# Performance work log

Measured on AMD Instinct MI355X. Metric: run time of the kernel, lower is better.

Reference implementation:

```python
import jax, jax.numpy as jnp
from jax import lax
import numpy as np

B, T, IN, H, OUT = 1024, 100, 64, 512, 64


def setup_inputs() -> dict:
    key = jax.random.key(0)
    ks = jax.random.split(key, 16)
    s_in = 1.0 / np.sqrt(IN)
    s_h = 1.0 / np.sqrt(H)
    inp = {
        'coeffs': jax.random.normal(ks[0], (B, T - 1, 4, IN), jnp.float32),
        'times': jnp.linspace(0.0, 1.0, T, dtype=jnp.float32),
        'dW': jax.random.normal(ks[1], (T - 1, B, H), jnp.float32),
        # initial_network: Linear(IN, H)
        'W_init': jax.random.normal(ks[2], (IN, H), jnp.float32) * s_in,
        'b_init': jnp.zeros((H,), jnp.float32),
        # drift MLP f: H -> H -> H
        'Wf1': jax.random.normal(ks[3], (H, H), jnp.float32) * s_h,
        'bf1': jnp.zeros((H,), jnp.float32),
        'Wf2': jax.random.normal(ks[4], (H, H), jnp.float32) * s_h,
        'bf2': jnp.zeros((H,), jnp.float32),
        # diffusion MLP g: H -> H -> H (tanh-bounded, diagonal noise)
        'Wg1': jax.random.normal(ks[5], (H, H), jnp.float32) * s_h,
        'bg1': jnp.zeros((H,), jnp.float32),
        'Wg2': jax.random.normal(ks[6], (H, H), jnp.float32) * s_h,
        'bg2': jnp.zeros((H,), jnp.float32),
        # readout: Tanh -> Linear(H,H) -> ReLU -> Linear(H,OUT)
        'Wl1': jax.random.normal(ks[7], (H, H), jnp.float32) * s_h,
        'bl1': jnp.zeros((H,), jnp.float32),
        'Wl2': jax.random.normal(ks[8], (H, OUT), jnp.float32) * s_h,
        'bl2': jnp.zeros((OUT,), jnp.float32),
    }
    return inp


def reference(coeffs, times, dW, W_init, b_init, Wf1, bf1, Wf2, bf2,
              Wg1, bg1, Wg2, bg2, Wl1, bl1, Wl2, bl2):
    # y0 = X.evaluate(times[0]) == constant coefficient of first spline segment
    x0 = coeffs[:, 0, 0, :]                      # [B, IN]
    y0 = x0 @ W_init + b_init                    # [B, H]

    def f(y):
        return jnp.tanh(y @ Wf1 + bf1) @ Wf2 + bf2

    def g(y):
        return jnp.tanh(jnp.tanh(y @ Wg1 + bg1) @ Wg2 + bg2)

    hs = times[1:] - times[:-1]                  # [T-1], equals dt on uniform grid

    def step(y, inp):
        h, dw = inp
        y_next = y + f(y) * h + g(y) * (jnp.sqrt(h) * dw)
        return y_next, y_next

    _, ys = lax.scan(step, y0, (hs, dW))         # ys: [T-1, B, H]
    z = jnp.concatenate([y0[None], ys], axis=0)  # [T, B, H]
    z = jnp.transpose(z, (1, 0, 2))              # [B, T, H]  (permute(1,0,2))

    # readout: Tanh -> Linear -> ReLU -> Linear
    out = jax.nn.relu(jnp.tanh(z) @ Wl1 + bl1) @ Wl2 + bl2  # [B, T, OUT]
    return out, z
```

## Files before the change

### kernel.cpp

```cpp
#include <hip/hip_runtime.h>
#include <hip/hip_bf16.h>
#include <math.h>

#define DEV __device__ __forceinline__

typedef __attribute__((ext_vector_type(8))) short short8;
typedef __attribute__((ext_vector_type(4))) float f32x4;
typedef __attribute__((ext_vector_type(4))) unsigned int u32x4;

static constexpr int Bsz  = 1024;
static constexpr int T    = 100;
static constexpr int TM1  = 99;
static constexpr int H    = 512;
static constexpr int OUTD = 64;
static constexpr int H2   = 1024;
static constexpr int BT   = Bsz * T;

DEV unsigned short f2bf(float f){
  unsigned int u = __float_as_uint(f);
  u += 0x7fffu + ((u >> 16) & 1u);
  return (unsigned short)(u >> 16);
}
DEV unsigned pack2(float lo, float hi){
  return (unsigned)f2bf(lo) | ((unsigned)f2bf(hi) << 16);
}
DEV float tanh_fast(float x){
  x = fminf(fmaxf(x, -15.f), 15.f);
  float e = __expf(2.f * x);
  return (e - 1.f) / (e + 1.f);
}

#define AISSUE(dst, p) asm volatile("global_load_dwordx4 %0, %1, off sc0 sc1" : "=&v"(dst) : "v"(p) : "memory")
#define PLOAD(dst, p)  asm volatile("global_load_dword %0, %1, off"          : "=&v"(dst) : "v"(p) : "memory")
#define SC_STORE(p, v) asm volatile("global_store_dword %0, %1, off sc0 sc1" :: "v"(p), "v"(v) : "memory")
#define VWAIT(n)       asm volatile("s_waitcnt vmcnt(" #n ")" ::: "memory"); __builtin_amdgcn_sched_barrier(0)

DEV void gbar(unsigned* cnt, unsigned target){
  __syncthreads();
  if (threadIdx.x == 0){
    __hip_atomic_fetch_add(cnt, 1u, __ATOMIC_RELAXED, __HIP_MEMORY_SCOPE_AGENT);
    while (__hip_atomic_load(cnt, __ATOMIC_RELAXED, __HIP_MEMORY_SCOPE_AGENT) < target)
      __builtin_amdgcn_s_sleep(1);
  }
  __syncthreads();
}

__global__ __launch_bounds__(256) void k_prep(const float* __restrict__ Wf1, const float* __restrict__ Wg1,
                                              const float* __restrict__ Wf2, const float* __restrict__ Wg2,
                                              const float* __restrict__ Wl1, const float* __restrict__ Wl2,
                                              unsigned short* __restrict__ W1T, unsigned short* __restrict__ W2T,
                                              unsigned short* __restrict__ Wl1F, unsigned short* __restrict__ Wl2F){
  __shared__ float tl[32][33];
  const float* src; unsigned short* dst; int N; int fmt;
  switch (blockIdx.z){
    case 0: src = Wf1; dst = W1T;             N = 512; fmt = 0; break;
    case 1: src = Wg1; dst = W1T + 512*512;   N = 512; fmt = 0; break;
    case 2: src = Wf2; dst = W2T;             N = 512; fmt = 0; break;
    case 3: src = Wg2; dst = W2T + 512*512;   N = 512; fmt = 0; break;
    case 4: src = Wl1; dst = Wl1F;            N = 512; fmt = 1; break;
    default: src = Wl2; dst = Wl2F;           N = 64;  fmt = 2; break;
  }
  int k0 = blockIdx.x*32, n0 = blockIdx.y*32;
  if (n0 >= N) return;
  int tx = threadIdx.x, ty = threadIdx.y;
  #pragma unroll
  for (int r = 0; r < 4; r++) tl[ty + r*8][tx] = src[(size_t)(k0 + ty + r*8) * N + n0 + tx];
  __syncthreads();
  if (fmt == 0){
    int kpos = k0 + ((tx & 15)*2 + (tx >> 4));
    #pragma unroll
    for (int r = 0; r < 4; r++) dst[(size_t)(n0 + ty + r*8) * 512 + kpos] = f2bf(tl[tx][ty + r*8]);
  } else {
    int k = k0 + tx;
    int Nc = (fmt == 1) ? 512 : 64;
    #pragma unroll
    for (int r = 0; r < 4; r++){
      int col = n0 + ty + r*8;
      size_t idx = (((size_t)(k >> 5)*Nc + col)*4 + ((k >> 3) & 3))*8 + (k & 7);
      dst[idx] = f2bf(tl[tx][ty + r*8]);
    }
  }
}

__global__ void k_zero(unsigned* __restrict__ cnts){
  cnts[threadIdx.x + blockIdx.x*256] = 0u;
}

#define KS1(K, W) \
  VWAIT(W); \
  { short8 a_ = *(short8*)&ap[(K)&7]; \
    p0 = __builtin_amdgcn_mfma_f32_16x16x32_bf16(a_, wb[(K)*2],   p0, 0,0,0); \
    p1 = __builtin_amdgcn_mfma_f32_16x16x32_bf16(a_, wb[(K)*2+1], p1, 0,0,0); } \
  if ((K) < 8) { AISSUE(ap[(K)&7], abase1 + (size_t)((K)+8)*65536); }

#define RUN16_P1 \
  AISSUE(ap[0], abase1);          AISSUE(ap[1], abase1+65536); \
  AISSUE(ap[2], abase1+131072);   AISSUE(ap[3], abase1+196608); \
  AISSUE(ap[4], abase1+262144);   AISSUE(ap[5], abase1+327680); \
  AISSUE(ap[6], abase1+393216);   AISSUE(ap[7], abase1+458752); \
  KS1( 0,7) KS1( 1,7) KS1( 2,7) KS1( 3,7) KS1( 4,7) KS1( 5,7) KS1( 6,7) KS1( 7,7) \
  KS1( 8,7) KS1( 9,6) KS1(10,5) KS1(11,4) KS1(12,3) KS1(13,2) KS1(14,1) KS1(15,0)

#define KS2(K, W) \
  VWAIT(W); \
  { short8 a_  = *(short8*)&ap[(K)&7]; \
    short8 b0_ = *(const short8*)(Wb2 + (K)*4096 + fr*64 + fq*16); \
    short8 b1_ = *(const short8*)(Wb2 + (K)*4096 + 1024 + fr*64 + fq*16); \
    q0 = __builtin_amdgcn_mfma_f32_16x16x32_bf16(a_, b0_, q0, 0,0,0); \
    q1 = __builtin_amdgcn_mfma_f32_16x16x32_bf16(a_, b1_, q1, 0,0,0); } \
  if ((K) < 8) { AISSUE(ap[(K)&7], abase2 + (size_t)((K)+8)*65536); }

#define RUN16_P2 \
  AISSUE(ap[0], abase2);          AISSUE(ap[1], abase2+65536); \
  AISSUE(ap[2], abase2+131072);   AISSUE(ap[3], abase2+196608); \
  AISSUE(ap[4], abase2+262144);   AISSUE(ap[5], abase2+327680); \
  AISSUE(ap[6], abase2+393216);   AISSUE(ap[7], abase2+458752); \
  KS2( 0,7) KS2( 1,7) KS2( 2,7) KS2( 3,7) KS2( 4,7) KS2( 5,7) KS2( 6,7) KS2( 7,7) \
  KS2( 8,7) KS2( 9,6) KS2(10,5) KS2(11,4) KS2(12,3) KS2(13,2) KS2(14,1) KS2(15,0)

__global__ __launch_bounds__(512, 1) void k_scan(
    const float* __restrict__ coeffs, const float* __restrict__ times,
    const float* __restrict__ dW,     const float* __restrict__ W_init,
    const float* __restrict__ b_init,
    const unsigned short* __restrict__ W1T, const unsigned short* __restrict__ W2T,
    const float* __restrict__ bf1, const float* __restrict__ bg1,
    const float* __restrict__ bf2, const float* __restrict__ bg2,
    unsigned short* __restrict__ ygk, unsigned short* __restrict__ uk,
    float* __restrict__ z, unsigned* __restrict__ cnts){
  __shared__ __align__(16) unsigned char W1s[65536];
  __shared__ __align__(16) unsigned char W2s[65536];
  __shared__ __align__(16) float cmb[64*68];
  __shared__ float tms[104];

  const int bid = blockIdx.x, mt = bid & 15, ns = bid >> 4;
  const int m0 = mt*64, n1 = ns*64, n2 = ns*32;
  const int tid = threadIdx.x, lane = tid & 63, w = tid >> 6;
  const int fr = lane & 15, fq = lane >> 4;
  const int band = w & 3, isg = w >> 2;
  unsigned* cnt = cnts + mt*32;
  unsigned ep = 0;

  #pragma unroll
  for (int i = 0; i < 8; i++){
    int u = i*512 + tid;
    int fqi = u & 3, cl = (u >> 2) & 63, kc = u >> 8;
    *(uint4*)(W1s + (size_t)u*16) = *(const uint4*)(W1T + (size_t)(n1+cl)*512 + kc*32 + fqi*8);
    const unsigned short* s2 = (cl < 32) ? (W2T + (size_t)(n2+cl)*512)
                                         : (W2T + (size_t)262144 + (size_t)(n2+cl-32)*512);
    *(uint4*)(W2s + (size_t)u*16) = *(const uint4*)(s2 + kc*32 + fqi*8);
  }
  if (tid < 100) tms[tid] = times[tid];
  { int row = tid >> 3, c0 = (tid & 7)*8;
    const float* src = coeffs + (size_t)(m0+row)*(TM1*4*64) + c0;
    *(float4*)(&cmb[row*68 + c0])     = *(const float4*)src;
    *(float4*)(&cmb[row*68 + c0 + 4]) = *(const float4*)(src + 4);
  }
  __syncthreads();

  short8 wb[32];
  #pragma unroll
  for (int kc = 0; kc < 16; ++kc){
    wb[kc*2]   = *(const short8*)(W1s + kc*4096 + isg*2048 +        fr*64 + fq*16);
    wb[kc*2+1] = *(const short8*)(W1s + kc*4096 + isg*2048 + 1024 + fr*64 + fq*16);
  }

  char* ygkb = (char*)ygk;
  char* ukb  = (char*)uk;
  const char* abase1 = ygkb + ((size_t)(m0 + band*16 + fr))*64 + fq*16;
  const char* abase2 = ukb + (size_t)isg*1048576 + ((size_t)(m0 + band*16 + fr))*64 + fq*16;
  char* ust = ukb  + ((size_t)((ns*2+isg)*1024 + m0 + band*16 + fq*4))*64 + fr*4;
  char* yst = ygkb + ((size_t)(ns*1024        + m0 + band*16 + fq*4))*64 + fr*4;
  const unsigned char* Wb2 = W2s + isg*2048;
  const float* dwb = dW + (size_t)(m0 + band*16 + fq*4)*512 + n2 + fr;
  float*       zb  = z  + ((size_t)(m0 + band*16 + fq*4)*T)*512 + n2 + fr;

  float yv[2][4];
  if (isg){
    #pragma unroll
    for (int r = 0; r < 4; r++){
      int row = band*16 + fq*4 + r;
      float s0 = b_init[n2 + fr], s1 = b_init[n2 + 16 + fr];
      #pragma unroll 8
      for (int k = 0; k < 64; k++){
        float xv = cmb[row*68 + k];
        s0 += xv * W_init[(size_t)k*512 + n2 + fr];
        s1 += xv * W_init[(size_t)k*512 + n2 + 16 + fr];
      }
      yv[0][r] = s0; yv[1][r] = s1;
      unsigned pv = pack2(s0, s1);
      SC_STORE(yst + r*64, pv);
      zb[(size_t)r*T*512]      = s0;
      zb[(size_t)r*T*512 + 16] = s1;
    }
    VWAIT(8);
  }
  ++ep; gbar(cnt, ep*16);

  const float b1v0 = ((n1 + isg*32 +      fr) < 512) ? bf1[n1 + isg*32 + fr]      : bg1[n1 + isg*32 + fr - 512];
  const float b1v1 = ((n1 + isg*32 + 16 + fr) < 512) ? bf1[n1 + isg*32 + 16 + fr] : bg1[n1 + isg*32 + 16 + fr - 512];
  const float b2v0 = isg ? bg2[n2 + fr]      : bf2[n2 + fr];
  const float b2v1 = isg ? bg2[n2 + 16 + fr] : bf2[n2 + 16 + fr];

  for (int t = 0; t < TM1; t++){
    float dv[8];
    {
      f32x4 p0 = {0.f,0.f,0.f,0.f}, p1 = {0.f,0.f,0.f,0.f};
      u32x4 ap[8];
      RUN16_P1;
      #pragma unroll
      for (int r = 0; r < 4; r++){
        unsigned pv = pack2(tanh_fast(p0[r] + b1v0), tanh_fast(p1[r] + b1v1));
        SC_STORE(ust + r*64, pv);
      }
      if (isg){
        const char* dp = (const char*)(dwb + (size_t)t*524288);
        PLOAD(dv[0], dp + 0);    PLOAD(dv[1], dp + 64);
        PLOAD(dv[2], dp + 2048); PLOAD(dv[3], dp + 2048+64);
        PLOAD(dv[4], dp + 4096); PLOAD(dv[5], dp + 4096+64);
        PLOAD(dv[6], dp + 6144); PLOAD(dv[7], dp + 6144+64);
        VWAIT(8);
      } else {
        VWAIT(0);
      }
    }
    ++ep; gbar(cnt, ep*16);

    {
      f32x4 q0 = {0.f,0.f,0.f,0.f}, q1 = {0.f,0.f,0.f,0.f};
      u32x4 ap[8];
      RUN16_P2;
      if (!isg){
        #pragma unroll
        for (int r = 0; r < 4; r++){
          int row = band*16 + fq*4 + r;
          cmb[row*68 + fr]      = q0[r] + b2v0;
          cmb[row*68 + 16 + fr] = q1[r] + b2v1;
        }
      }
      __syncthreads();
      if (isg){
        float h  = tms[t+1] - tms[t];
        float sq = sqrtf(h);
        #pragma unroll
        for (int r = 0; r < 4; r++){
          int row = band*16 + fq*4 + r;
          float f0 = cmb[row*68 + fr],        f1 = cmb[row*68 + 16 + fr];
          float g0 = tanh_fast(q0[r] + b2v0), g1 = tanh_fast(q1[r] + b2v1);
          float y0n = yv[0][r] + f0*h + g0*(sq*dv[r*2]);
          float y1n = yv[1][r] + f1*h + g1*(sq*dv[r*2+1]);
          yv[0][r] = y0n; yv[1][r] = y1n;
          unsigned pv = pack2(y0n, y1n);
          SC_STORE(yst + r*64, pv);
          zb[(size_t)r*T*512 + (size_t)(t+1)*512]      = y0n;
          zb[(size_t)r*T*512 + (size_t)(t+1)*512 + 16] = y1n;
        }
        VWAIT(8);
      }
    }
    if (t < TM1-1){ ++ep; gbar(cnt, ep*16); }
  }
}

__global__ __launch_bounds__(512, 1) void k_read(
    const float* __restrict__ z, const unsigned short* __restrict__ Wl1F,
    const float* __restrict__ bl1, const unsigned short* __restrict__ Wl2F,
    const float* __restrict__ bl2, float* __restrict__ out){
  __shared__ __align__(16) unsigned char zt[65536];
  __shared__ __align__(16) unsigned char relF[65536];
  const int tid = threadIdx.x, lane = tid & 63, w = tid >> 6;
  const int fr = lane & 15, fq = lane >> 4;
  const size_t rr0 = (size_t)blockIdx.x * 64;
  const int cw = w * 64;

  { int row = tid >> 3, c0 = (tid & 7) * 64;
    const float* zr = z + (rr0 + row) * 512 + c0;
    #pragma unroll
    for (int j = 0; j < 2; ++j){
      int kc = (c0 >> 5) + j;
      #pragma unroll
      for (int f = 0; f < 4; ++f){
        float4 v0 = *(const float4*)(zr + j*32 + f*8);
        float4 v1 = *(const float4*)(zr + j*32 + f*8 + 4);
        unsigned d0 = pack2(tanh_fast(v0.x), tanh_fast(v0.y));
        unsigned d1 = pack2(tanh_fast(v0.z), tanh_fast(v0.w));
        unsigned d2 = pack2(tanh_fast(v1.x), tanh_fast(v1.y));
        unsigned d3 = pack2(tanh_fast(v1.z), tanh_fast(v1.w));
        uint4 pk = {d0, d1, d2, d3};
        *(uint4*)(zt + (size_t)((kc*64 + row)*4 + f)*16) = pk;
      }
    }
  }
  __syncthreads();

  f32x4 acc[4][4];
  #pragma unroll
  for (int m = 0; m < 4; m++)
    #pragma unroll
    for (int c = 0; c < 4; c++) acc[m][c] = (f32x4){0.f,0.f,0.f,0.f};
  for (int kc = 0; kc < 16; ++kc){
    short8 a[4];
    #pragma unroll
    for (int m = 0; m < 4; m++)
      a[m] = *(const short8*)(zt + (size_t)((kc*64 + m*16 + fr)*4 + fq)*16);
    #pragma unroll
    for (int c = 0; c < 4; c++){
      short8 b = *(const short8*)(Wl1F + (((size_t)kc*512 + cw + c*16 + fr)*4 + fq)*8);
      #pragma unroll
      for (int m = 0; m < 4; m++)
        acc[m][c] = __builtin_amdgcn_mfma_f32_16x16x32_bf16(a[m], b, acc[m][c], 0, 0, 0);
    }
  }
  float bl1v[4];
  #pragma unroll
  for (int c = 0; c < 4; c++) bl1v[c] = bl1[cw + c*16 + fr];

  #pragma unroll
  for (int h = 0; h < 2; ++h){
    __syncthreads();
    if ((w >> 2) == h){
      float* stg = (float*)zt;
      int cb = cw - h*256;
      #pragma unroll
      for (int m = 0; m < 4; m++)
        #pragma unroll
        for (int c = 0; c < 4; c++)
          #pragma unroll
          for (int r = 0; r < 4; r++)
            stg[(m*16 + fq*4 + r)*256 + cb + c*16 + fr] = fmaxf(acc[m][c][r] + bl1v[c], 0.f);
    }
    __syncthreads();
    { int row = tid >> 3, c8 = (tid & 7) * 32;
      const float* stg = (const float*)zt;
      int kc = h*8 + (tid & 7);
      #pragma unroll
      for (int f = 0; f < 4; ++f){
        const float* p = stg + row*256 + c8 + f*8;
        unsigned d0 = pack2(p[0], p[1]);
        unsigned d1 = pack2(p[2], p[3]);
        unsigned d2 = pack2(p[4], p[5]);
        unsigned d3 = pack2(p[6], p[7]);
        uint4 pk = {d0, d1, d2, d3};
        *(uint4*)(relF + (size_t)((kc*64 + row)*4 + f)*16) = pk;
      }
    }
  }
  __syncthreads();

  f32x4 acc2[2];
  acc2[0] = (f32x4){0.f,0.f,0.f,0.f};
  acc2[1] = (f32x4){0.f,0.f,0.f,0.f};
  const int mt2 = w & 3, ocb = (w >> 2) * 32;
  for (int kc = 0; kc < 16; ++kc){
    short8 a = *(const short8*)(relF + (size_t)((kc*64 + mt2*16 + fr)*4 + fq)*16);
    #pragma unroll
    for (int j = 0; j < 2; j++){
      short8 b = *(const short8*)(Wl2F + (((size_t)(kc*64 + ocb + j*16 + fr))*4 + fq)*8);
      acc2[j] = __builtin_amdgcn_mfma_f32_16x16x32_bf16(a, b, acc2[j], 0, 0, 0);
    }
  }
  #pragma unroll
  for (int j = 0; j < 2; j++){
    #pragma unroll
    for (int r = 0; r < 4; r++){
      int row = mt2*16 + fq*4 + r;
      int oc  = ocb + j*16 + fr;
      out[(rr0 + row)*64 + oc] = acc2[j][r] + bl2[oc];
    }
  }
}

extern "C" void kernel_launch(void* const* d_in, const int* in_sizes, int n_in,
                              void* d_out, int out_size, void* d_ws, size_t ws_size,
                              hipStream_t stream){
  (void)in_sizes; (void)n_in; (void)out_size; (void)ws_size;
  const float* coeffs = (const float*)d_in[0];
  const float* times  = (const float*)d_in[1];
  const float* dW     = (const float*)d_in[2];
  const float* W_init = (const float*)d_in[3];
  const float* b_init = (const float*)d_in[4];
  const float* Wf1 = (const float*)d_in[5];
  const float* bf1 = (const float*)d_in[6];
  const float* Wf2 = (const float*)d_in[7];
  const float* bf2 = (const float*)d_in[8];
  const float* Wg1 = (const float*)d_in[9];
  const float* bg1 = (const float*)d_in[10];
  const float* Wg2 = (const float*)d_in[11];
  const float* bg2 = (const float*)d_in[12];
  const float* Wl1 = (const float*)d_in[13];
  const float* bl1 = (const float*)d_in[14];
  const float* Wl2 = (const float*)d_in[15];
  const float* bl2 = (const float*)d_in[16];

  float* out = (float*)d_out;
  float* z   = out + (size_t)Bsz * T * OUTD;

  char* wsp = (char*)d_ws;
  auto carve = [&](size_t bytes) -> void* {
    void* p = (void*)wsp; wsp += (bytes + 255) & ~(size_t)255; return p;
  };
  unsigned short* W1T  = (unsigned short*)carve((size_t)H2 * H * 2);
  unsigned short* W2T  = (unsigned short*)carve((size_t)H2 * H * 2);
  unsigned short* Wl1F = (unsigned short*)carve((size_t)H * H * 2);
  unsigned short* Wl2F = (unsigned short*)carve((size_t)OUTD * H * 2);
  unsigned short* ygk  = (unsigned short*)carve((size_t)Bsz * H * 2);
  unsigned short* uk   = (unsigned short*)carve((size_t)Bsz * H2 * 2);
  unsigned*       cnts = (unsigned*)carve(16 * 32 * sizeof(unsigned));

  k_zero<<<dim3(2), 256, 0, stream>>>(cnts);
  k_prep<<<dim3(16, 16, 6), dim3(32, 8), 0, stream>>>(Wf1, Wg1, Wf2, Wg2, Wl1, Wl2,
                                                      W1T, W2T, Wl1F, Wl2F);
  k_scan<<<dim3(256), 512, 0, stream>>>(coeffs, times, dW, W_init, b_init,
                                        W1T, W2T, bf1, bg1, bf2, bg2,
                                        ygk, uk, z, cnts);
  k_read<<<dim3(BT / 64), 512, 0, stream>>>(z, Wl1F, bl1, Wl2F, bl2, out);
}
```

Measured before the change: 1.140 ms.

## Replace block-wide grid barriers with per-wave counters and split row crews

Replaces the block-level global barrier in the persistent scan kernel with per-wavefront arrive/poll counters. The 64 rows of each block are split into two independent 32-row crews that synchronise separately, so one crew can start its next phase while the other finishes. The f/g combine now uses an LDS flag handshake between waves instead of __syncthreads. W1 is read from LDS per step instead of being held in registers, which frees VGPRs but adds LDS traffic. The aim is to cut barrier latency and stagger the two matmul phases, at the cost of more subtle memory-ordering requirements on the relaxed atomics.

```diff
diff --git a/kernel.cpp b/kernel.cpp
--- a/kernel.cpp
+++ b/kernel.cpp
@@ -35,14 +35,13 @@
 #define SC_STORE(p, v) asm volatile("global_store_dword %0, %1, off sc0 sc1" :: "v"(p), "v"(v) : "memory")
 #define VWAIT(n)       asm volatile("s_waitcnt vmcnt(" #n ")" ::: "memory"); __builtin_amdgcn_sched_barrier(0)
 
-DEV void gbar(unsigned* cnt, unsigned target){
-  __syncthreads();
-  if (threadIdx.x == 0){
-    __hip_atomic_fetch_add(cnt, 1u, __ATOMIC_RELAXED, __HIP_MEMORY_SCOPE_AGENT);
-    while (__hip_atomic_load(cnt, __ATOMIC_RELAXED, __HIP_MEMORY_SCOPE_AGENT) < target)
-      __builtin_amdgcn_s_sleep(1);
-  }
-  __syncthreads();
+DEV void poll_ge(unsigned* c, unsigned tgt){
+  while (__hip_atomic_load(c, __ATOMIC_RELAXED, __HIP_MEMORY_SCOPE_AGENT) < tgt)
+    __builtin_amdgcn_s_sleep(1);
+}
+DEV void arrive(unsigned* c){
+  if ((threadIdx.x & 63) == 0)
+    __hip_atomic_fetch_add(c, 1u, __ATOMIC_RELAXED, __HIP_MEMORY_SCOPE_AGENT);
 }
 
 __global__ __launch_bounds__(256) void k_prep(const float* __restrict__ Wf1, const float* __restrict__ Wg1,
@@ -86,37 +85,22 @@
   cnts[threadIdx.x + blockIdx.x*256] = 0u;
 }
 
-#define KS1(K, W) \
-  VWAIT(W); \
-  { short8 a_ = *(short8*)&ap[(K)&7]; \
-    p0 = __builtin_amdgcn_mfma_f32_16x16x32_bf16(a_, wb[(K)*2],   p0, 0,0,0); \
-    p1 = __builtin_amdgcn_mfma_f32_16x16x32_bf16(a_, wb[(K)*2+1], p1, 0,0,0); } \
-  if ((K) < 8) { AISSUE(ap[(K)&7], abase1 + (size_t)((K)+8)*65536); }
-
-#define RUN16_P1 \
-  AISSUE(ap[0], abase1);          AISSUE(ap[1], abase1+65536); \
-  AISSUE(ap[2], abase1+131072);   AISSUE(ap[3], abase1+196608); \
-  AISSUE(ap[4], abase1+262144);   AISSUE(ap[5], abase1+327680); \
-  AISSUE(ap[6], abase1+393216);   AISSUE(ap[7], abase1+458752); \
-  KS1( 0,7) KS1( 1,7) KS1( 2,7) KS1( 3,7) KS1( 4,7) KS1( 5,7) KS1( 6,7) KS1( 7,7) \
-  KS1( 8,7) KS1( 9,6) KS1(10,5) KS1(11,4) KS1(12,3) KS1(13,2) KS1(14,1) KS1(15,0)
-
-#define KS2(K, W) \
+#define KSX(K, W) \
   VWAIT(W); \
   { short8 a_  = *(short8*)&ap[(K)&7]; \
-    short8 b0_ = *(const short8*)(Wb2 + (K)*4096 + fr*64 + fq*16); \
-    short8 b1_ = *(const short8*)(Wb2 + (K)*4096 + 1024 + fr*64 + fq*16); \
-    q0 = __builtin_amdgcn_mfma_f32_16x16x32_bf16(a_, b0_, q0, 0,0,0); \
-    q1 = __builtin_amdgcn_mfma_f32_16x16x32_bf16(a_, b1_, q1, 0,0,0); } \
-  if ((K) < 8) { AISSUE(ap[(K)&7], abase2 + (size_t)((K)+8)*65536); }
-
-#define RUN16_P2 \
-  AISSUE(ap[0], abase2);          AISSUE(ap[1], abase2+65536); \
-  AISSUE(ap[2], abase2+131072);   AISSUE(ap[3], abase2+196608); \
-  AISSUE(ap[4], abase2+262144);   AISSUE(ap[5], abase2+327680); \
-  AISSUE(ap[6], abase2+393216);   AISSUE(ap[7], abase2+458752); \
-  KS2( 0,7) KS2( 1,7) KS2( 2,7) KS2( 3,7) KS2( 4,7) KS2( 5,7) KS2( 6,7) KS2( 7,7) \
-  KS2( 8,7) KS2( 9,6) KS2(10,5) KS2(11,4) KS2(12,3) KS2(13,2) KS2(14,1) KS2(15,0)
+    short8 b0_ = *(const short8*)(wbp + (K)*4096); \
+    short8 b1_ = *(const short8*)(wbp + (K)*4096 + 1024); \
+    p0 = __builtin_amdgcn_mfma_f32_16x16x32_bf16(a_, b0_, p0, 0,0,0); \
+    p1 = __builtin_amdgcn_mfma_f32_16x16x32_bf16(a_, b1_, p1, 0,0,0); } \
+  if ((K) < 8) { AISSUE(ap[(K)&7], abp + (size_t)((K)+8)*65536); }
+
+#define RUN16X \
+  AISSUE(ap[0], abp);          AISSUE(ap[1], abp+65536); \
+  AISSUE(ap[2], abp+131072);   AISSUE(ap[3], abp+196608); \
+  AISSUE(ap[4], abp+262144);   AISSUE(ap[5], abp+327680); \
+  AISSUE(ap[6], abp+393216);   AISSUE(ap[7], abp+458752); \
+  KSX( 0,7) KSX( 1,7) KSX( 2,7) KSX( 3,7) KSX( 4,7) KSX( 5,7) KSX( 6,7) KSX( 7,7) \
+  KSX( 8,7) KSX( 9,6) KSX(10,5) KSX(11,4) KSX(12,3) KSX(13,2) KSX(14,1) KSX(15,0)
 
 __global__ __launch_bounds__(512, 1) void k_scan(
     const float* __restrict__ coeffs, const float* __restrict__ times,
@@ -129,16 +113,17 @@
     float* __restrict__ z, unsigned* __restrict__ cnts){
   __shared__ __align__(16) unsigned char W1s[65536];
   __shared__ __align__(16) unsigned char W2s[65536];
-  __shared__ __align__(16) float cmb[64*68];
+  __shared__ float cmb[2][32][33];
+  __shared__ float x0s[64][66];
   __shared__ float tms[104];
-
-  const int bid = blockIdx.x, mt = bid & 15, ns = bid >> 4;
-  const int m0 = mt*64, n1 = ns*64, n2 = ns*32;
+  __shared__ unsigned fflag[4];
+
+  const int bid = blockIdx.x, pair = bid & 15, ns = bid >> 4;
+  const int m0 = pair*64, n1 = ns*64, n2 = ns*32;
   const int tid = threadIdx.x, lane = tid & 63, w = tid >> 6;
   const int fr = lane & 15, fq = lane >> 4;
-  const int band = w & 3, isg = w >> 2;
-  unsigned* cnt = cnts + mt*32;
-  unsigned ep = 0;
+  const int crew = w >> 2, v = w & 3, band = v & 1, hr = v >> 1;
+  const int rbase = m0 + crew*32 + band*16;
 
   #pragma unroll
   for (int i = 0; i < 8; i++){
@@ -150,114 +135,130 @@
     *(uint4*)(W2s + (size_t)u*16) = *(const uint4*)(s2 + kc*32 + fqi*8);
   }
   if (tid < 100) tms[tid] = times[tid];
+  if (tid < 4)  fflag[tid] = 0u;
   { int row = tid >> 3, c0 = (tid & 7)*8;
     const float* src = coeffs + (size_t)(m0+row)*(TM1*4*64) + c0;
-    *(float4*)(&cmb[row*68 + c0])     = *(const float4*)src;
-    *(float4*)(&cmb[row*68 + c0 + 4]) = *(const float4*)(src + 4);
+    *(float4*)(&x0s[row][c0])     = *(const float4*)src;
+    *(float4*)(&x0s[row][c0 + 4]) = *(const float4*)(src + 4);
   }
   __syncthreads();
 
-  short8 wb[32];
-  #pragma unroll
-  for (int kc = 0; kc < 16; ++kc){
-    wb[kc*2]   = *(const short8*)(W1s + kc*4096 + isg*2048 +        fr*64 + fq*16);
-    wb[kc*2+1] = *(const short8*)(W1s + kc*4096 + isg*2048 + 1024 + fr*64 + fq*16);
-  }
+  unsigned* cbase = cnts + pair*64;
+  unsigned* c1own = cbase + crew*16;
+  unsigned* c1oth = cbase + (1-crew)*16;
+  unsigned* c2own = cbase + 32 + crew*16;
 
   char* ygkb = (char*)ygk;
   char* ukb  = (char*)uk;
-  const char* abase1 = ygkb + ((size_t)(m0 + band*16 + fr))*64 + fq*16;
-  const char* abase2 = ukb + (size_t)isg*1048576 + ((size_t)(m0 + band*16 + fr))*64 + fq*16;
-  char* ust = ukb  + ((size_t)((ns*2+isg)*1024 + m0 + band*16 + fq*4))*64 + fr*4;
-  char* yst = ygkb + ((size_t)(ns*1024        + m0 + band*16 + fq*4))*64 + fr*4;
-  const unsigned char* Wb2 = W2s + isg*2048;
-  const float* dwb = dW + (size_t)(m0 + band*16 + fq*4)*512 + n2 + fr;
-  float*       zb  = z  + ((size_t)(m0 + band*16 + fq*4)*T)*512 + n2 + fr;
+  const char* ab1 = ygkb + ((size_t)(rbase + fr))*64 + fq*16;
+  const char* ab2 = ukb + (size_t)hr*1048576 + ((size_t)(rbase + fr))*64 + fq*16;
+  char* up = ukb  + (size_t)(ns*2 + hr)*65536 + ((size_t)(rbase + fq*4))*64 + fr*4;
+  char* yp = ygkb + (size_t)ns*65536          + ((size_t)(rbase + fq*4))*64 + fr*4;
+  const unsigned char* wbp1 = W1s + (hr*32 + fr)*64 + fq*16;
+  const unsigned char* wbp2 = W2s + (hr*32 + fr)*64 + fq*16;
+  float* zp = z + ((size_t)(rbase + fq*4))*T*512 + n2 + fr;
+
+  const float* b1src = (ns < 8) ? bf1 : bg1;
+  const int    b1off = n1 - ((ns < 8) ? 0 : 512) + hr*32 + fr;
+  const float b1v0 = b1src[b1off], b1v1 = b1src[b1off + 16];
+  const float* b2src = hr ? bg2 : bf2;
+  const float b2v0 = b2src[n2 + fr], b2v1 = b2src[n2 + 16 + fr];
 
   float yv[2][4];
-  if (isg){
+  if (hr == 1){
     #pragma unroll
     for (int r = 0; r < 4; r++){
-      int row = band*16 + fq*4 + r;
+      int lrow = crew*32 + band*16 + fq*4 + r;
       float s0 = b_init[n2 + fr], s1 = b_init[n2 + 16 + fr];
       #pragma unroll 8
       for (int k = 0; k < 64; k++){
-        float xv = cmb[row*68 + k];
+        float xv = x0s[lrow][k];
         s0 += xv * W_init[(size_t)k*512 + n2 + fr];
         s1 += xv * W_init[(size_t)k*512 + n2 + 16 + fr];
       }
       yv[0][r] = s0; yv[1][r] = s1;
-      unsigned pv = pack2(s0, s1);
-      SC_STORE(yst + r*64, pv);
-      zb[(size_t)r*T*512]      = s0;
-      zb[(size_t)r*T*512 + 16] = s1;
+      SC_STORE(yp + r*64, pack2(s0, s1));
+    }
+    #pragma unroll
+    for (int r = 0; r < 4; r++){
+      zp[(size_t)r*T*512]      = yv[0][r];
+      zp[(size_t)r*T*512 + 16] = yv[1][r];
     }
     VWAIT(8);
-  }
-  ++ep; gbar(cnt, ep*16);
-
-  const float b1v0 = ((n1 + isg*32 +      fr) < 512) ? bf1[n1 + isg*32 + fr]      : bg1[n1 + isg*32 + fr - 512];
-  const float b1v1 = ((n1 + isg*32 + 16 + fr) < 512) ? bf1[n1 + isg*32 + 16 + fr] : bg1[n1 + isg*32 + 16 + fr - 512];
-  const float b2v0 = isg ? bg2[n2 + fr]      : bf2[n2 + fr];
-  const float b2v1 = isg ? bg2[n2 + 16 + fr] : bf2[n2 + 16 + fr];
-
+    arrive(c2own);
+  }
+
+  float dv[8];
   for (int t = 0; t < TM1; t++){
-    float dv[8];
+    VWAIT(0);
+    poll_ge(c2own, 32u*(unsigned)(t+1));
+    poll_ge(c1oth, 64u*(unsigned)t + 64u*(unsigned)crew);
+
     {
       f32x4 p0 = {0.f,0.f,0.f,0.f}, p1 = {0.f,0.f,0.f,0.f};
       u32x4 ap[8];
-      RUN16_P1;
+      const char* abp = ab1;
+      const unsigned char* wbp = wbp1;
+      RUN16X;
       #pragma unroll
-      for (int r = 0; r < 4; r++){
-        unsigned pv = pack2(tanh_fast(p0[r] + b1v0), tanh_fast(p1[r] + b1v1));
-        SC_STORE(ust + r*64, pv);
-      }
-      if (isg){
-        const char* dp = (const char*)(dwb + (size_t)t*524288);
-        PLOAD(dv[0], dp + 0);    PLOAD(dv[1], dp + 64);
-        PLOAD(dv[2], dp + 2048); PLOAD(dv[3], dp + 2048+64);
-        PLOAD(dv[4], dp + 4096); PLOAD(dv[5], dp + 4096+64);
-        PLOAD(dv[6], dp + 6144); PLOAD(dv[7], dp + 6144+64);
+      for (int r = 0; r < 4; r++)
+        SC_STORE(up + r*64, pack2(tanh_fast(p0[r] + b1v0), tanh_fast(p1[r] + b1v1)));
+      if (hr == 1){
+        const char* dp = (const char*)dW + (((size_t)t*1024 + rbase + fq*4)*512 + n2 + fr)*4;
+        PLOAD(dv[0], dp + 0);      PLOAD(dv[1], dp + 64);
+        PLOAD(dv[2], dp + 2048);   PLOAD(dv[3], dp + 2048+64);
+        PLOAD(dv[4], dp + 4096);   PLOAD(dv[5], dp + 4096+64);
+        PLOAD(dv[6], dp + 6144);   PLOAD(dv[7], dp + 6144+64);
         VWAIT(8);
       } else {
         VWAIT(0);
       }
     }
-    ++ep; gbar(cnt, ep*16);
+    arrive(c1own);
+
+    poll_ge(c1own, 64u*(unsigned)(t+1));
 
     {
-      f32x4 q0 = {0.f,0.f,0.f,0.f}, q1 = {0.f,0.f,0.f,0.f};
+      f32x4 p0 = {0.f,0.f,0.f,0.f}, p1 = {0.f,0.f,0.f,0.f};
       u32x4 ap[8];
-      RUN16_P2;
-      if (!isg){
+      const char* abp = ab2;
+      const unsigned char* wbp = wbp2;
+      RUN16X;
+      if (hr == 0){
         #pragma unroll
         for (int r = 0; r < 4; r++){
-          int row = band*16 + fq*4 + r;
-          cmb[row*68 + fr]      = q0[r] + b2v0;
-          cmb[row*68 + 16 + fr] = q1[r] + b2v1;
+          int lrow = band*16 + fq*4 + r;
+          cmb[crew][lrow][fr]      = p0[r] + b2v0;
+          cmb[crew][lrow][fr + 16] = p1[r] + b2v1;
         }
-      }
-      __syncthreads();
-      if (isg){
+        __hip_atomic_store(&fflag[crew*2 + band], (unsigned)(t+1),
+                           __ATOMIC_RELEASE, __HIP_MEMORY_SCOPE_WORKGROUP);
+      } else {
+        while (__hip_atomic_load(&fflag[crew*2 + band], __ATOMIC_ACQUIRE,
+                                 __HIP_MEMORY_SCOPE_WORKGROUP) < (unsigned)(t+1)) {}
         float h  = tms[t+1] - tms[t];
         float sq = sqrtf(h);
+        float zn0[4], zn1[4];
         #pragma unroll
         for (int r = 0; r < 4; r++){
-          int row = band*16 + fq*4 + r;
-          float f0 = cmb[row*68 + fr],        f1 = cmb[row*68 + 16 + fr];
-          float g0 = tanh_fast(q0[r] + b2v0), g1 = tanh_fast(q1[r] + b2v1);
+          int lrow = band*16 + fq*4 + r;
+          float f0 = cmb[crew][lrow][fr], f1 = cmb[crew][lrow][fr + 16];
+          float g0 = tanh_fast(p0[r] + b2v0), g1 = tanh_fast(p1[r] + b2v1);
           float y0n = yv[0][r] + f0*h + g0*(sq*dv[r*2]);
           float y1n = yv[1][r] + f1*h + g1*(sq*dv[r*2+1]);
           yv[0][r] = y0n; yv[1][r] = y1n;
-          unsigned pv = pack2(y0n, y1n);
-          SC_STORE(yst + r*64, pv);
-          zb[(size_t)r*T*512 + (size_t)(t+1)*512]      = y0n;
-          zb[(size_t)r*T*512 + (size_t)(t+1)*512 + 16] = y1n;
+          zn0[r] = y0n; zn1[r] = y1n;
+          SC_STORE(yp + r*64, pack2(y0n, y1n));
+        }
+        #pragma unroll
+        for (int r = 0; r < 4; r++){
+          zp[(size_t)r*T*512 + (size_t)(t+1)*512]      = zn0[r];
+          zp[(size_t)r*T*512 + (size_t)(t+1)*512 + 16] = zn1[r];
         }
         VWAIT(8);
+        arrive(c2own);
       }
     }
-    if (t < TM1-1){ ++ep; gbar(cnt, ep*16); }
   }
 }
 
@@ -404,9 +405,9 @@
   unsigned short* Wl2F = (unsigned short*)carve((size_t)OUTD * H * 2);
   unsigned short* ygk  = (unsigned short*)carve((size_t)Bsz * H * 2);
   unsigned short* uk   = (unsigned short*)carve((size_t)Bsz * H2 * 2);
-  unsigned*       cnts = (unsigned*)carve(16 * 32 * sizeof(unsigned));
-
-  k_zero<<<dim3(2), 256, 0, stream>>>(cnts);
+  unsigned*       cnts = (unsigned*)carve(1024 * sizeof(unsigned));
+
+  k_zero<<<dim3(4), 256, 0, stream>>>(cnts);
   k_prep<<<dim3(16, 16, 6), dim3(32, 8), 0, stream>>>(Wf1, Wg1, Wf2, Wg2, Wl1, Wl2,
                                                       W1T, W2T, Wl1F, Wl2F);
   k_scan<<<dim3(256), 512, 0, stream>>>(coeffs, times, dW, W_init, b_init,
```

After: 2.722 ms. +138.7%, slower.

## Give each timestep its own exchange buffer so loads can skip system-coherent caching

Applied to the files above, without the earlier changes.

When the workspace is large enough, the scan kernel writes the per-step bf16 hidden state and activations to a separate slot for every timestep. Because no address is ever rewritten, the A-operand loads can use L2-coherent loads (sc0 only) and no longer need the sc0 sc1 loads that bypass caches. Phase 1 also reads the W1 B-operand from LDS each step instead of holding it in 32 registers, which frees VGPRs but adds LDS traffic. The change uses far more workspace (about 130 MB of per-step buffers), which adds write footprint. It keeps a fallback template for small workspaces.

```diff
diff --git a/kernel.cpp b/kernel.cpp
--- a/kernel.cpp
+++ b/kernel.cpp
@@ -30,7 +30,8 @@
   return (e - 1.f) / (e + 1.f);
 }
 
-#define AISSUE(dst, p) asm volatile("global_load_dwordx4 %0, %1, off sc0 sc1" : "=&v"(dst) : "v"(p) : "memory")
+#define AISSUE_CC(dst, p) asm volatile("global_load_dwordx4 %0, %1, off sc0 sc1" : "=&v"(dst) : "v"(p) : "memory")
+#define AISSUE_L2(dst, p) asm volatile("global_load_dwordx4 %0, %1, off sc0"     : "=&v"(dst) : "v"(p) : "memory")
 #define PLOAD(dst, p)  asm volatile("global_load_dword %0, %1, off"          : "=&v"(dst) : "v"(p) : "memory")
 #define SC_STORE(p, v) asm volatile("global_store_dword %0, %1, off sc0 sc1" :: "v"(p), "v"(v) : "memory")
 #define VWAIT(n)       asm volatile("s_waitcnt vmcnt(" #n ")" ::: "memory"); __builtin_amdgcn_sched_barrier(0)
@@ -86,38 +87,26 @@
   cnts[threadIdx.x + blockIdx.x*256] = 0u;
 }
 
-#define KS1(K, W) \
-  VWAIT(W); \
-  { short8 a_ = *(short8*)&ap[(K)&7]; \
-    p0 = __builtin_amdgcn_mfma_f32_16x16x32_bf16(a_, wb[(K)*2],   p0, 0,0,0); \
-    p1 = __builtin_amdgcn_mfma_f32_16x16x32_bf16(a_, wb[(K)*2+1], p1, 0,0,0); } \
-  if ((K) < 8) { AISSUE(ap[(K)&7], abase1 + (size_t)((K)+8)*65536); }
-
-#define RUN16_P1 \
-  AISSUE(ap[0], abase1);          AISSUE(ap[1], abase1+65536); \
-  AISSUE(ap[2], abase1+131072);   AISSUE(ap[3], abase1+196608); \
-  AISSUE(ap[4], abase1+262144);   AISSUE(ap[5], abase1+327680); \
-  AISSUE(ap[6], abase1+393216);   AISSUE(ap[7], abase1+458752); \
-  KS1( 0,7) KS1( 1,7) KS1( 2,7) KS1( 3,7) KS1( 4,7) KS1( 5,7) KS1( 6,7) KS1( 7,7) \
-  KS1( 8,7) KS1( 9,6) KS1(10,5) KS1(11,4) KS1(12,3) KS1(13,2) KS1(14,1) KS1(15,0)
-
-#define KS2(K, W) \
+#define KSX(K, W, LD) \
   VWAIT(W); \
   { short8 a_  = *(short8*)&ap[(K)&7]; \
-    short8 b0_ = *(const short8*)(Wb2 + (K)*4096 + fr*64 + fq*16); \
-    short8 b1_ = *(const short8*)(Wb2 + (K)*4096 + 1024 + fr*64 + fq*16); \
-    q0 = __builtin_amdgcn_mfma_f32_16x16x32_bf16(a_, b0_, q0, 0,0,0); \
-    q1 = __builtin_amdgcn_mfma_f32_16x16x32_bf16(a_, b1_, q1, 0,0,0); } \
-  if ((K) < 8) { AISSUE(ap[(K)&7], abase2 + (size_t)((K)+8)*65536); }
-
-#define RUN16_P2 \
-  AISSUE(ap[0], abase2);          AISSUE(ap[1], abase2+65536); \
-  AISSUE(ap[2], abase2+131072);   AISSUE(ap[3], abase2+196608); \
-  AISSUE(ap[4], abase2+262144);   AISSUE(ap[5], abase2+327680); \
-  AISSUE(ap[6], abase2+393216);   AISSUE(ap[7], abase2+458752); \
-  KS2( 0,7) KS2( 1,7) KS2( 2,7) KS2( 3,7) KS2( 4,7) KS2( 5,7) KS2( 6,7) KS2( 7,7) \
-  KS2( 8,7) KS2( 9,6) KS2(10,5) KS2(11,4) KS2(12,3) KS2(13,2) KS2(14,1) KS2(15,0)
-
+    short8 b0_ = *(const short8*)(wbp + (K)*4096); \
+    short8 b1_ = *(const short8*)(wbp + (K)*4096 + 1024); \
+    p0 = __builtin_amdgcn_mfma_f32_16x16x32_bf16(a_, b0_, p0, 0,0,0); \
+    p1 = __builtin_amdgcn_mfma_f32_16x16x32_bf16(a_, b1_, p1, 0,0,0); } \
+  if ((K) < 8) { LD(ap[(K)&7], abp + (size_t)((K)+8)*65536); }
+
+#define RUN16X(LD) \
+  LD(ap[0], abp);          LD(ap[1], abp+65536); \
+  LD(ap[2], abp+131072);   LD(ap[3], abp+196608); \
+  LD(ap[4], abp+262144);   LD(ap[5], abp+327680); \
+  LD(ap[6], abp+393216);   LD(ap[7], abp+458752); \
+  KSX( 0,7,LD) KSX( 1,7,LD) KSX( 2,7,LD) KSX( 3,7,LD) \
+  KSX( 4,7,LD) KSX( 5,7,LD) KSX( 6,7,LD) KSX( 7,7,LD) \
+  KSX( 8,7,LD) KSX( 9,6,LD) KSX(10,5,LD) KSX(11,4,LD) \
+  KSX(12,3,LD) KSX(13,2,LD) KSX(14,1,LD) KSX(15,0,LD)
+
+template<int UNIQ>
 __global__ __launch_bounds__(512, 1) void k_scan(
     const float* __restrict__ coeffs, const float* __restrict__ times,
     const float* __restrict__ dW,     const float* __restrict__ W_init,
@@ -132,6 +121,9 @@
   __shared__ __align__(16) float cmb[64*68];
   __shared__ float tms[104];
 
+  constexpr size_t YB = UNIQ ? (size_t)Bsz * H  * 2 : 0;
+  constexpr size_t UB = UNIQ ? (size_t)Bsz * H2 * 2 : 0;
+
   const int bid = blockIdx.x, mt = bid & 15, ns = bid >> 4;
   const int m0 = mt*64, n1 = ns*64, n2 = ns*32;
   const int tid = threadIdx.x, lane = tid & 63, w = tid >> 6;
@@ -157,67 +149,61 @@
   }
   __syncthreads();
 
-  short8 wb[32];
-  #pragma unroll
-  for (int kc = 0; kc < 16; ++kc){
-    wb[kc*2]   = *(const short8*)(W1s + kc*4096 + isg*2048 +        fr*64 + fq*16);
-    wb[kc*2+1] = *(const short8*)(W1s + kc*4096 + isg*2048 + 1024 + fr*64 + fq*16);
-  }
-
   char* ygkb = (char*)ygk;
   char* ukb  = (char*)uk;
-  const char* abase1 = ygkb + ((size_t)(m0 + band*16 + fr))*64 + fq*16;
-  const char* abase2 = ukb + (size_t)isg*1048576 + ((size_t)(m0 + band*16 + fr))*64 + fq*16;
-  char* ust = ukb  + ((size_t)((ns*2+isg)*1024 + m0 + band*16 + fq*4))*64 + fr*4;
-  char* yst = ygkb + ((size_t)(ns*1024        + m0 + band*16 + fq*4))*64 + fr*4;
-  const unsigned char* Wb2 = W2s + isg*2048;
-  const float* dwb = dW + (size_t)(m0 + band*16 + fq*4)*512 + n2 + fr;
-  float*       zb  = z  + ((size_t)(m0 + band*16 + fq*4)*T)*512 + n2 + fr;
+  const char* ab1 = ygkb + ((size_t)(m0 + band*16 + fr))*64 + fq*16;
+  const char* ab2 = ukb + (size_t)isg*1048576 + ((size_t)(m0 + band*16 + fr))*64 + fq*16;
+  char* up = ukb  + (size_t)(ns*2 + isg)*65536 + ((size_t)(m0 + band*16 + fq*4))*64 + fr*4;
+  char* yp = ygkb + (size_t)ns*65536           + ((size_t)(m0 + band*16 + fq*4))*64 + fr*4;
+  const unsigned char* wbp1 = W1s + isg*2048 + fr*64 + fq*16;
+  const unsigned char* wbp2 = W2s + isg*2048 + fr*64 + fq*16;
+  float* zp = z + ((size_t)(m0 + band*16 + fq*4))*T*512 + n2 + fr;
+
+  const float* b1src = (ns < 8) ? bf1 : bg1;
+  const int    b1off = n1 - ((ns < 8) ? 0 : 512) + isg*32 + fr;
+  const float b1v0 = b1src[b1off], b1v1 = b1src[b1off + 16];
+  const float* b2src = isg ? bg2 : bf2;
+  const float b2v0 = b2src[n2 + fr], b2v1 = b2src[n2 + 16 + fr];
 
   float yv[2][4];
   if (isg){
     #pragma unroll
     for (int r = 0; r < 4; r++){
-      int row = band*16 + fq*4 + r;
+      int lrow = band*16 + fq*4 + r;
       float s0 = b_init[n2 + fr], s1 = b_init[n2 + 16 + fr];
       #pragma unroll 8
       for (int k = 0; k < 64; k++){
-        float xv = cmb[row*68 + k];
+        float xv = cmb[lrow*68 + k];
         s0 += xv * W_init[(size_t)k*512 + n2 + fr];
         s1 += xv * W_init[(size_t)k*512 + n2 + 16 + fr];
       }
       yv[0][r] = s0; yv[1][r] = s1;
-      unsigned pv = pack2(s0, s1);
-      SC_STORE(yst + r*64, pv);
-      zb[(size_t)r*T*512]      = s0;
-      zb[(size_t)r*T*512 + 16] = s1;
+      SC_STORE(yp + r*64, pack2(s0, s1));
+      zp[(size_t)r*T*512]      = s0;
+      zp[(size_t)r*T*512 + 16] = s1;
     }
     VWAIT(8);
   }
   ++ep; gbar(cnt, ep*16);
-
-  const float b1v0 = ((n1 + isg*32 +      fr) < 512) ? bf1[n1 + isg*32 + fr]      : bg1[n1 + isg*32 + fr - 512];
-  const float b1v1 = ((n1 + isg*32 + 16 + fr) < 512) ? bf1[n1 + isg*32 + 16 + fr] : bg1[n1 + isg*32 + 16 + fr - 512];
-  const float b2v0 = isg ? bg2[n2 + fr]      : bf2[n2 + fr];
-  const float b2v1 = isg ? bg2[n2 + 16 + fr] : bf2[n2 + 16 + fr];
 
   for (int t = 0; t < TM1; t++){
     float dv[8];
     {
       f32x4 p0 = {0.f,0.f,0.f,0.f}, p1 = {0.f,0.f,0.f,0.f};
       u32x4 ap[8];
-      RUN16_P1;
+      const char* abp = ab1 + (size_t)t*YB;
+      const unsigned char* wbp = wbp1;
+      if constexpr (UNIQ) { RUN16X(AISSUE_L2); } else { RUN16X(AISSUE_CC); }
+      char* upt = up + (size_t)t*UB;
       #pragma unroll
-      for (int r = 0; r < 4; r++){
-        unsigned pv = pack2(tanh_fast(p0[r] + b1v0), tanh_fast(p1[r] + b1v1));
-        SC_STORE(ust + r*64, pv);
-      }
+      for (int r = 0; r < 4; r++)
+        SC_STORE(upt + r*64, pack2(tanh_fast(p0[r] + b1v0), tanh_fast(p1[r] + b1v1)));
       if (isg){
-        const char* dp = (const char*)(dwb + (size_t)t*524288);
-        PLOAD(dv[0], dp + 0);    PLOAD(dv[1], dp + 64);
-        PLOAD(dv[2], dp + 2048); PLOAD(dv[3], dp + 2048+64);
-        PLOAD(dv[4], dp + 4096); PLOAD(dv[5], dp + 4096+64);
-        PLOAD(dv[6], dp + 6144); PLOAD(dv[7], dp + 6144+64);
+        const char* dp = (const char*)dW + (((size_t)t*1024 + m0 + band*16 + fq*4)*512 + n2 + fr)*4;
+        PLOAD(dv[0], dp + 0);      PLOAD(dv[1], dp + 64);
+        PLOAD(dv[2], dp + 2048);   PLOAD(dv[3], dp + 2048+64);
+        PLOAD(dv[4], dp + 4096);   PLOAD(dv[5], dp + 4096+64);
+        PLOAD(dv[6], dp + 6144);   PLOAD(dv[7], dp + 6144+64);
         VWAIT(8);
       } else {
         VWAIT(0);
@@ -226,33 +212,35 @@
     ++ep; gbar(cnt, ep*16);
 
     {
-      f32x4 q0 = {0.f,0.f,0.f,0.f}, q1 = {0.f,0.f,0.f,0.f};
+      f32x4 p0 = {0.f,0.f,0.f,0.f}, p1 = {0.f,0.f,0.f,0.f};
       u32x4 ap[8];
-      RUN16_P2;
+      const char* abp = ab2 + (size_t)t*UB;
+      const unsigned char* wbp = wbp2;
+      if constexpr (UNIQ) { RUN16X(AISSUE_L2); } else { RUN16X(AISSUE_CC); }
       if (!isg){
         #pragma unroll
         for (int r = 0; r < 4; r++){
-          int row = band*16 + fq*4 + r;
-          cmb[row*68 + fr]      = q0[r] + b2v0;
-          cmb[row*68 + 16 + fr] = q1[r] + b2v1;
+          int lrow = band*16 + fq*4 + r;
+          cmb[lrow*68 + fr]      = p0[r] + b2v0;
+          cmb[lrow*68 + 16 + fr] = p1[r] + b2v1;
         }
       }
       __syncthreads();
       if (isg){
         float h  = tms[t+1] - tms[t];
         float sq = sqrtf(h);
+        char* ypt = yp + (size_t)(t+1)*YB;
         #pragma unroll
         for (int r = 0; r < 4; r++){
-          int row = band*16 + fq*4 + r;
-          float f0 = cmb[row*68 + fr],        f1 = cmb[row*68 + 16 + fr];
-          float g0 = tanh_fast(q0[r] + b2v0), g1 = tanh_fast(q1[r] + b2v1);
+          int lrow = band*16 + fq*4 + r;
+          float f0 = cmb[lrow*68 + fr],       f1 = cmb[lrow*68 + 16 + fr];
+          float g0 = tanh_fast(p0[r] + b2v0), g1 = tanh_fast(p1[r] + b2v1);
           float y0n = yv[0][r] + f0*h + g0*(sq*dv[r*2]);
           float y1n = yv[1][r] + f1*h + g1*(sq*dv[r*2+1]);
           yv[0][r] = y0n; yv[1][r] = y1n;
-          unsigned pv = pack2(y0n, y1n);
-          SC_STORE(yst + r*64, pv);
-          zb[(size_t)r*T*512 + (size_t)(t+1)*512]      = y0n;
-          zb[(size_t)r*T*512 + (size_t)(t+1)*512 + 16] = y1n;
+          SC_STORE(ypt + r*64, pack2(y0n, y1n));
+          zp[(size_t)r*T*512 + (size_t)(t+1)*512]      = y0n;
+          zp[(size_t)r*T*512 + (size_t)(t+1)*512 + 16] = y1n;
         }
         VWAIT(8);
       }
@@ -372,7 +360,7 @@
 extern "C" void kernel_launch(void* const* d_in, const int* in_sizes, int n_in,
                               void* d_out, int out_size, void* d_ws, size_t ws_size,
                               hipStream_t stream){
-  (void)in_sizes; (void)n_in; (void)out_size; (void)ws_size;
+  (void)in_sizes; (void)n_in; (void)out_size;
   const float* coeffs = (const float*)d_in[0];
   const float* times  = (const float*)d_in[1];
   const float* dW     = (const float*)d_in[2];
@@ -394,6 +382,8 @@
   float* out = (float*)d_out;
   float* z   = out + (size_t)Bsz * T * OUTD;
 
+  const bool full = ws_size >= ((size_t)320 << 20);
+
   char* wsp = (char*)d_ws;
   auto carve = [&](size_t bytes) -> void* {
     void* p = (void*)wsp; wsp += (bytes + 255) & ~(size_t)255; return p;
@@ -402,15 +392,22 @@
   unsigned short* W2T  = (unsigned short*)carve((size_t)H2 * H * 2);
   unsigned short* Wl1F = (unsigned short*)carve((size_t)H * H * 2);
   unsigned short* Wl2F = (unsigned short*)carve((size_t)OUTD * H * 2);
-  unsigned short* ygk  = (unsigned short*)carve((size_t)Bsz * H * 2);
-  unsigned short* uk   = (unsigned short*)carve((size_t)Bsz * H2 * 2);
-  unsigned*       cnts = (unsigned*)carve(16 * 32 * sizeof(unsigned));
-
-  k_zero<<<dim3(2), 256, 0, stream>>>(cnts);
+  unsigned short* ygk  = (unsigned short*)carve(full ? (size_t)T   * Bsz * H  * 2
+                                                     : (size_t)Bsz * H  * 2);
+  unsigned short* uk   = (unsigned short*)carve(full ? (size_t)TM1 * Bsz * H2 * 2
+                                                     : (size_t)Bsz * H2 * 2);
+  unsigned*       cnts = (unsigned*)carve(1024 * sizeof(unsigned));
+
+  k_zero<<<dim3(4), 256, 0, stream>>>(cnts);
   k_prep<<<dim3(16, 16, 6), dim3(32, 8), 0, stream>>>(Wf1, Wg1, Wf2, Wg2, Wl1, Wl2,
                                                       W1T, W2T, Wl1F, Wl2F);
-  k_scan<<<dim3(256), 512, 0, stream>>>(coeffs, times, dW, W_init, b_init,
-                                        W1T, W2T, bf1, bg1, bf2, bg2,
-                                        ygk, uk, z, cnts);
+  if (full)
+    k_scan<1><<<dim3(256), 512, 0, stream>>>(coeffs, times, dW, W_init, b_init,
+                                             W1T, W2T, bf1, bg1, bf2, bg2,
+                                             ygk, uk, z, cnts);
+  else
+    k_scan<0><<<dim3(256), 512, 0, stream>>>(coeffs, times, dW, W_init, b_init,
+                                             W1T, W2T, bf1, bg1, bf2, bg2,
+                                             ygk, uk, z, cnts);
   k_read<<<dim3(BT / 64), 512, 0, stream>>>(z, Wl1F, bl1, Wl2F, bl2, out);
 }
```

After: 937.2 us. 1.22x faster.
